# Optimization experiments

Measured on AMD Instinct MI355X. Metric: run time of the kernel, lower is better.

The kernel has to match this reference:

```python
import jax, jax.numpy as jnp
import numpy as np

D_MODEL = 1024
NUM_HEAD = 16
D_K = D_MODEL // NUM_HEAD
B, S = 2, 2048


def setup_inputs() -> dict:
    key = jax.random.key(0)
    ks = jax.random.split(key, 12)
    s = 1.0 / np.sqrt(D_MODEL)
    return {
        "x_q": jax.random.normal(ks[0], (B, S, D_MODEL), jnp.float32),
        "x_k": jax.random.normal(ks[1], (B, S, D_MODEL), jnp.float32),
        "x_v": jax.random.normal(ks[2], (B, S, D_MODEL), jnp.float32),
        "mask": jax.random.randint(ks[3], (B, S, S), 0, 2, jnp.int32),
        "Wq": jax.random.uniform(ks[4], (D_MODEL, D_MODEL), jnp.float32, -s, s),
        "bq": jax.random.uniform(ks[5], (D_MODEL,), jnp.float32, -s, s),
        "Wk": jax.random.uniform(ks[6], (D_MODEL, D_MODEL), jnp.float32, -s, s),
        "bk": jax.random.uniform(ks[7], (D_MODEL,), jnp.float32, -s, s),
        "Wv": jax.random.uniform(ks[8], (D_MODEL, D_MODEL), jnp.float32, -s, s),
        "bv": jax.random.uniform(ks[9], (D_MODEL,), jnp.float32, -s, s),
        "Wo": jax.random.uniform(ks[10], (D_MODEL, D_MODEL), jnp.float32, -s, s),
        "bo": jax.random.uniform(ks[11], (D_MODEL,), jnp.float32, -s, s),
    }


def reference(x_q, x_k, x_v, mask, Wq, bq, Wk, bk, Wv, bv, Wo, bo):
    # projections -> [B, H, S, d_k]
    def proj(x, W, b):
        y = x @ W.T + b
        return y.reshape(B, -1, NUM_HEAD, D_K).transpose(0, 2, 1, 3)

    q = proj(x_q, Wq, bq)
    k = proj(x_k, Wk, bk)
    v = proj(x_v, Wv, bv)
    scale = 1.0 / np.sqrt(D_K).astype(np.float32)
    scores = jnp.einsum("bhqd,bhkd->bhqk", q, k) * scale
    scores = jnp.where(mask[:, None, :, :] == 0, jnp.float32(-1e9), scores)
    p = jax.nn.softmax(scores, axis=-1)  # dropout is identity in eval mode
    attn = jnp.einsum("bhqk,bhkd->bhqd", p, v)
    concat = attn.transpose(0, 2, 1, 3).reshape(B, S, D_MODEL)
    return concat @ Wo.T + bo
```

## Files before the change

kernel.cpp:

```cpp
#include <hip/hip_runtime.h>
#include <cstdint>
#include <cstddef>

#define D_MODELX 1024
#define NUM_HEADX 16
#define D_KX 64
#define BBX 2
#define SSX 2048
#define M_TOK 4096
#define MBYTE (1u << 20)

typedef __attribute__((ext_vector_type(8))) short short8;
typedef __attribute__((ext_vector_type(4))) short short4v;
typedef __attribute__((ext_vector_type(4))) float float4v;
typedef __attribute__((ext_vector_type(2))) unsigned uint2v;
typedef __attribute__((ext_vector_type(4))) unsigned uint4v;

__device__ __forceinline__ short f2bf(float f) {
  unsigned u = __builtin_bit_cast(unsigned, f);
  u = u + 0x7FFFu + ((u >> 16) & 1u);
  return (short)(u >> 16);
}

__global__ void mask_bits_kernel(const int* __restrict__ mask, unsigned* __restrict__ mbits) {
  int i = blockIdx.x * blockDim.x + threadIdx.x;
  bool v = mask[i] != 0;
  unsigned long long bal = __ballot(v);
  int lane = threadIdx.x & 63;
  if (lane == 0)       mbits[i >> 5] = (unsigned)bal;
  else if (lane == 32) mbits[i >> 5] = (unsigned)(bal >> 32);
}

__global__ void cvt_w4_kernel(const float* __restrict__ w0, const float* __restrict__ w1,
                              const float* __restrict__ w2, const float* __restrict__ w3,
                              short* __restrict__ o0, short* __restrict__ o1,
                              short* __restrict__ o2, short* __restrict__ o3) {
  int z = blockIdx.y;
  const float* in = (z == 0) ? w0 : (z == 1) ? w1 : (z == 2) ? w2 : w3;
  short* out = (z == 0) ? o0 : (z == 1) ? o1 : (z == 2) ? o2 : o3;
  int i = blockIdx.x * blockDim.x + threadIdx.x;
  float4v v = ((const float4v*)in)[i];
  short4v s;
  s[0] = f2bf(v[0]); s[1] = f2bf(v[1]); s[2] = f2bf(v[2]); s[3] = f2bf(v[3]);
  ((short4v*)out)[i] = s;
}

__global__ void cvt_x3_kernel(const float* __restrict__ x0, const float* __restrict__ x1,
                              const float* __restrict__ x2,
                              short* __restrict__ o0, short* __restrict__ o1,
                              short* __restrict__ o2) {
  int z = blockIdx.y;
  const float* in = (z == 0) ? x0 : (z == 1) ? x1 : x2;
  short* out = (z == 0) ? o0 : (z == 1) ? o1 : o2;
  int i = blockIdx.x * blockDim.x + threadIdx.x;
  float4v v = ((const float4v*)in)[i];
  short4v s;
  s[0] = f2bf(v[0]); s[1] = f2bf(v[1]); s[2] = f2bf(v[2]); s[3] = f2bf(v[3]);
  ((short4v*)out)[i] = s;
}

#define GBK 64

__device__ __forceinline__ void gemm_body(const short* __restrict__ A,
                                          const short* __restrict__ Bw,
                                          const float* __restrict__ bias,
                                          float oscale, void* __restrict__ outp, int mode) {
  __shared__ short lds_a[128 * 64];
  __shared__ short lds_b[128 * 64];
  const int tid = threadIdx.x;
  const int lane = tid & 63;
  const int wid = tid >> 6;
  const int wm = wid >> 1, wn = wid & 1;
  const int bn = blockIdx.x, bm = blockIdx.y;
  const int l15 = lane & 15, lg = lane >> 4;

  const int s_row = tid >> 3;
  const int s_cB = ((tid & 7) << 4) ^ ((s_row & 7) << 4);
  const short* Abase = A + (size_t)(bm * 128) * 1024 + (s_cB >> 1);
  const short* Bbase = Bw + (size_t)(bn * 128) * 1024 + (s_cB >> 1);

  const int xmask = (l15 & 7) << 4;
  const int a_b0 = (wm * 64 + l15) * 128 + ((lg * 16) ^ xmask);
  const int a_b1 = (wm * 64 + l15) * 128 + ((64 + lg * 16) ^ xmask);
  const int b_b0 = (wn * 64 + l15) * 128 + ((lg * 16) ^ xmask);
  const int b_b1 = (wn * 64 + l15) * 128 + ((64 + lg * 16) ^ xmask);

  float4v acc[4][4];
#pragma unroll
  for (int m = 0; m < 4; ++m)
#pragma unroll
    for (int n = 0; n < 4; ++n) acc[m][n] = (float4v){0.f, 0.f, 0.f, 0.f};

  for (int kt = 0; kt < 1024; kt += GBK) {
#pragma unroll
    for (int it = 0; it < 4; ++it) {
      int row = it * 32 + s_row;
      __builtin_amdgcn_global_load_lds(
          (const uint32_t*)(Abase + (size_t)row * 1024 + kt),
          (uint32_t*)(lds_a + (it * 256 + wid * 64) * 8), 16, 0, 0);
      __builtin_amdgcn_global_load_lds(
          (const uint32_t*)(Bbase + (size_t)row * 1024 + kt),
          (uint32_t*)(lds_b + (it * 256 + wid * 64) * 8), 16, 0, 0);
    }
    __syncthreads();

    short8 af[4][2];
#pragma unroll
    for (int m = 0; m < 4; ++m) {
      af[m][0] = *(const short8*)((const char*)lds_a + a_b0 + m * 2048);
      af[m][1] = *(const short8*)((const char*)lds_a + a_b1 + m * 2048);
    }
#pragma unroll
    for (int n = 0; n < 4; ++n) {
      short8 b0 = *(const short8*)((const char*)lds_b + b_b0 + n * 2048);
      short8 b1 = *(const short8*)((const char*)lds_b + b_b1 + n * 2048);
#pragma unroll
      for (int m = 0; m < 4; ++m) {
        acc[m][n] = __builtin_amdgcn_mfma_f32_16x16x32_bf16(af[m][0], b0, acc[m][n], 0, 0, 0);
        acc[m][n] = __builtin_amdgcn_mfma_f32_16x16x32_bf16(af[m][1], b1, acc[m][n], 0, 0, 0);
      }
    }
    __syncthreads();
  }

#pragma unroll
  for (int n = 0; n < 4; ++n) {
    int col = bn * 128 + wn * 64 + n * 16 + l15;
    float bv = bias[col];
#pragma unroll
    for (int m = 0; m < 4; ++m) {
      if (mode == 2) {
        int base_row = bm * 128 + wm * 64 + m * 16 + lg * 4;
        int bidx = base_row >> 11, s = base_row & 2047;
        int h = col >> 6, d = col & 63;
        short4v sv;
#pragma unroll
        for (int r = 0; r < 4; ++r) sv[r] = f2bf(acc[m][n][r] + bv);
        *(short4v*)&((short*)outp)[(((size_t)(bidx * NUM_HEADX + h)) * D_KX + d) * SSX + s] = sv;
      } else {
#pragma unroll
        for (int r = 0; r < 4; ++r) {
          int row = bm * 128 + wm * 64 + m * 16 + lg * 4 + r;
          float val = (acc[m][n][r] + bv) * oscale;
          if (mode == 0) {
            int bidx = row >> 11, s = row & 2047;
            int h = col >> 6, d = col & 63;
            ((short*)outp)[(((size_t)(bidx * NUM_HEADX + h)) * SSX + s) * D_KX + d] = f2bf(val);
          } else {
            ((float*)outp)[(size_t)row * D_MODELX + col] = val;
          }
        }
      }
    }
  }
}

__global__ __launch_bounds__(256) void gemm_qkv_kernel(
    const short* __restrict__ xq, const short* __restrict__ xk, const short* __restrict__ xv,
    const short* __restrict__ wq, const short* __restrict__ wk, const short* __restrict__ wv,
    const float* __restrict__ bq, const float* __restrict__ bk, const float* __restrict__ bv,
    short* __restrict__ qo, short* __restrict__ ko, short* __restrict__ vo, float qs) {
  int z = blockIdx.z;
  const short* A = (z == 0) ? xq : (z == 1) ? xk : xv;
  const short* W = (z == 0) ? wq : (z == 1) ? wk : wv;
  const float* bi = (z == 0) ? bq : (z == 1) ? bk : bv;
  void* out = (z == 0) ? (void*)qo : (z == 1) ? (void*)ko : (void*)vo;
  float os = (z == 0) ? qs : 1.0f;
  int mode = (z == 2) ? 2 : 0;
  gemm_body(A, W, bi, os, out, mode);
}

__global__ __launch_bounds__(256) void gemm_one_kernel(const short* __restrict__ A,
                                                       const short* __restrict__ W,
                                                       const float* __restrict__ bias,
                                                       float os, void* __restrict__ out, int mode) {
  gemm_body(A, W, bias, os, out, mode);
}

__global__ __launch_bounds__(256, 3) void attn_kernel(const short* __restrict__ q_ws,
                                                      const short* __restrict__ k_ws,
                                                      const short* __restrict__ vT_ws,
                                                      const unsigned* __restrict__ mbits,
                                                      short* __restrict__ attn_ws,
                                                      short* __restrict__ opart,
                                                      float* __restrict__ lpart) {
  __shared__ short k_lds[2][4096];
  __shared__ short vT_lds[2][4096];
  __shared__ short p_lds[4][2048];

  const int tid = threadIdx.x;
  const int lane = tid & 63;
  const int w = tid >> 6;
  const int l15 = lane & 15, lg = lane >> 4;
  const int bid0 = blockIdx.x;
  const int bid = ((bid0 & 7) << 6) | (bid0 >> 3);
  const int qt = bid & 15;
  const int bh = bid >> 4;
  const int b = bh >> 4;
  const int h = bh & 15;
  const int z = blockIdx.z;
  const int nsplit = gridDim.z;
  const int nt = (SSX / 64) / nsplit;
  const int kb0 = z * nt * 64;

  const int qrow = qt * 128 + w * 32;

  const int xm15 = (l15 & 7) << 4;
  const int rd_c0 = l15 * 128 + ((lg * 16) ^ xm15);
  const int rd_c1 = l15 * 128 + ((64 + lg * 16) ^ xm15);
  char* kbase = (char*)k_lds;
  char* vbase = (char*)vT_lds;
  char* pwave = (char*)p_lds[w];
  const int s8 = ((l15 >> 2) & 3) << 3;
  const int pw_off = l15 * 32 + ((lg * 8) ^ s8);
  const int pr0 = (lg >> 1) * 512 + l15 * 32 + (((lg & 1) * 16) ^ s8);
  const int pr1 = pr0 ^ 8;

  const int srow = tid >> 2;
  const int scolS = (tid & 3) * 16;
  const int st0 = srow * 128 + ((scolS * 2) ^ ((srow & 7) << 4));
  const int st1 = srow * 128 + ((scolS * 2 + 16) ^ ((srow & 7) << 4));

  const short* kp = k_ws + (size_t)bh * SSX * D_KX + (size_t)srow * D_KX + scolS;
  const short* vp = vT_ws + (size_t)bh * D_KX * SSX + (size_t)srow * SSX + scolS;

  short8 qf[2][2];
#pragma unroll
  for (int qg = 0; qg < 2; ++qg)
#pragma unroll
    for (int c = 0; c < 2; ++c)
      qf[qg][c] = *(const short8*)(q_ws + ((size_t)bh * SSX + qrow + qg * 16 + l15) * D_KX + c * 32 + lg * 8);

  float4v acc[2][4];
#pragma unroll
  for (int qg = 0; qg < 2; ++qg)
#pragma unroll
    for (int db = 0; db < 4; ++db) acc[qg][db] = (float4v){0.f, 0.f, 0.f, 0.f};
  float l_part[2] = {0.f, 0.f};

  short8 kr0, kr1, vr0, vr1;
  auto loadt = [&](int kb) {
    const short* kq = kp + (size_t)kb * D_KX;
    kr0 = *(const short8*)kq;
    kr1 = *(const short8*)(kq + 8);
    const short* vq = vp + kb;
    vr0 = *(const short8*)vq;
    vr1 = *(const short8*)(vq + 8);
  };
  auto storet = [&](int BUF) {
    *(short8*)(kbase + BUF + st0) = kr0;
    *(short8*)(kbase + BUF + st1) = kr1;
    *(short8*)(vbase + BUF + st0) = vr0;
    *(short8*)(vbase + BUF + st1) = vr1;
  };

  const unsigned* mrow0 = mbits + ((size_t)b * SSX + qrow + l15) * (SSX / 32) + (kb0 >> 5);
  const unsigned* mrow1 = mbits + ((size_t)b * SSX + qrow + 16 + l15) * (SSX / 32) + (kb0 >> 5);
  unsigned long long mw0 = *(const unsigned long long*)mrow0, mwn0 = 0;
  unsigned long long mw1 = *(const unsigned long long*)mrow1, mwn1 = 0;

  loadt(kb0);
  storet(0);
  loadt(kb0 + 64);
  __syncthreads();

  auto step = [&](int t, int CURB, int NXTB) {
    float p[2][4][4];
#pragma unroll
    for (int kf = 0; kf < 4; ++kf) {
      short8 k0 = *(const short8*)(kbase + CURB + rd_c0 + kf * 2048);
      short8 k1 = *(const short8*)(kbase + CURB + rd_c1 + kf * 2048);
      float4v f0 = (float4v){0.f, 0.f, 0.f, 0.f};
      f0 = __builtin_amdgcn_mfma_f32_16x16x32_bf16(k0, qf[0][0], f0, 0, 0, 0);
      f0 = __builtin_amdgcn_mfma_f32_16x16x32_bf16(k1, qf[0][1], f0, 0, 0, 0);
      float4v f1 = (float4v){0.f, 0.f, 0.f, 0.f};
      f1 = __builtin_amdgcn_mfma_f32_16x16x32_bf16(k0, qf[1][0], f1, 0, 0, 0);
      f1 = __builtin_amdgcn_mfma_f32_16x16x32_bf16(k1, qf[1][1], f1, 0, 0, 0);
#pragma unroll
      for (int r = 0; r < 4; ++r) { p[0][kf][r] = f0[r]; p[1][kf][r] = f1[r]; }
    }

    if (t < nt - 1) storet(NXTB);
    if (t < nt - 2) loadt(kb0 + (t + 2) * 64);
    if (t < nt - 1) {
      mwn0 = *(const unsigned long long*)(mrow0 + 2 * (t + 1));
      mwn1 = *(const unsigned long long*)(mrow1 + 2 * (t + 1));
    }

#pragma unroll
    for (int qg = 0; qg < 2; ++qg) {
      unsigned long long sh = (qg == 0 ? mw0 : mw1) >> (lg * 4);
      unsigned mlo = (unsigned)sh, mhi = (unsigned)(sh >> 32);
      float tsum = 0.f;
#pragma unroll
      for (int kf = 0; kf < 4; ++kf) {
        float pv_[4];
#pragma unroll
        for (int r = 0; r < 4; ++r) {
          float pv = __builtin_amdgcn_exp2f(p[qg][kf][r]);
          unsigned bit = (kf < 2 ? mlo : mhi) & (1u << ((kf & 1) * 16 + r));
          pv_[r] = bit ? pv : 0.0f;
        }
        tsum += (pv_[0] + pv_[1]) + (pv_[2] + pv_[3]);
        unsigned u0, u1;
        asm("v_cvt_pk_bf16_f32 %0, %1, %2" : "=v"(u0) : "v"(pv_[0]), "v"(pv_[1]));
        asm("v_cvt_pk_bf16_f32 %0, %1, %2" : "=v"(u1) : "v"(pv_[2]), "v"(pv_[3]));
        *(uint2v*)(pwave + pw_off + qg * 2048 + kf * 512) = (uint2v){u0, u1};
      }
      l_part[qg] += tsum;
    }

    short8 pa[2][2];
#pragma unroll
    for (int qg = 0; qg < 2; ++qg)
#pragma unroll
      for (int c = 0; c < 2; ++c) {
        uint2v a0 = *(const uint2v*)(pwave + pr0 + qg * 2048 + c * 1024);
        uint2v a1 = *(const uint2v*)(pwave + pr1 + qg * 2048 + c * 1024);
        pa[qg][c] = __builtin_bit_cast(short8, (uint4v){a0[0], a0[1], a1[0], a1[1]});
      }

#pragma unroll
    for (int db = 0; db < 4; ++db) {
      short8 vb0 = *(const short8*)(vbase + CURB + rd_c0 + db * 2048);
      short8 vb1 = *(const short8*)(vbase + CURB + rd_c1 + db * 2048);
#pragma unroll
      for (int qg = 0; qg < 2; ++qg) {
        acc[qg][db] = __builtin_amdgcn_mfma_f32_16x16x32_bf16(vb0, pa[qg][0], acc[qg][db], 0, 0, 0);
        acc[qg][db] = __builtin_amdgcn_mfma_f32_16x16x32_bf16(vb1, pa[qg][1], acc[qg][db], 0, 0, 0);
      }
    }

    __syncthreads();
    mw0 = mwn0;
    mw1 = mwn1;
  };

  for (int t2 = 0; t2 < nt / 2; ++t2) {
    step(2 * t2, 0, 8192);
    step(2 * t2 + 1, 8192, 0);
  }

#pragma unroll
  for (int qg = 0; qg < 2; ++qg) {
    float lp = l_part[qg];
    lp += __shfl_xor(lp, 16);
    lp += __shfl_xor(lp, 32);
    const int q = qrow + qg * 16 + l15;
    if (nsplit == 1) {
      float inv = 1.0f / lp;
      size_t ttok = (size_t)b * SSX + q;
#pragma unroll
      for (int db = 0; db < 4; ++db) {
        short4v sv;
#pragma unroll
        for (int r = 0; r < 4; ++r) sv[r] = f2bf(acc[qg][db][r] * inv);
        *(short4v*)&attn_ws[ttok * D_MODELX + h * 64 + db * 16 + lg * 4] = sv;
      }
    } else {
      size_t rowp = ((size_t)z * 32 + bh) * SSX + q;
      if (lg == 0) lpart[rowp] = lp;
#pragma unroll
      for (int db = 0; db < 4; ++db) {
        short4v sv;
#pragma unroll
        for (int r = 0; r < 4; ++r) sv[r] = f2bf(acc[qg][db][r]);
        *(short4v*)&opart[rowp * D_KX + db * 16 + lg * 4] = sv;
      }
    }
  }
}

__global__ void combine_kernel(const short* __restrict__ opart, const float* __restrict__ lpart,
                               short* __restrict__ attn_ws) {
  int gtid = blockIdx.x * blockDim.x + threadIdx.x;
  int row = gtid >> 3;
  int dc = (gtid & 7) * 8;
  int bh = row >> 11, s = row & 2047;
  int b = bh >> 4, h = bh & 15;
  float inv = 1.0f / (lpart[row] + lpart[row + 32 * SSX]);
  short8 o0 = *(const short8*)&opart[(size_t)row * D_KX + dc];
  short8 o1 = *(const short8*)&opart[((size_t)row + 32 * SSX) * D_KX + dc];
  short8 sv;
#pragma unroll
  for (int j = 0; j < 8; ++j) {
    float f0 = __builtin_bit_cast(float, ((unsigned)(unsigned short)o0[j]) << 16);
    float f1 = __builtin_bit_cast(float, ((unsigned)(unsigned short)o1[j]) << 16);
    sv[j] = f2bf((f0 + f1) * inv);
  }
  *(short8*)&attn_ws[(((size_t)b * SSX + s) * D_MODELX) + h * 64 + dc] = sv;
}

extern "C" void kernel_launch(void* const* d_in, const int* in_sizes, int n_in,
                              void* d_out, int out_size, void* d_ws, size_t ws_size,
                              hipStream_t stream) {
  const float* x_q = (const float*)d_in[0];
  const float* x_k = (const float*)d_in[1];
  const float* x_v = (const float*)d_in[2];
  const int*   mask = (const int*)d_in[3];
  const float* Wq = (const float*)d_in[4];
  const float* bq = (const float*)d_in[5];
  const float* Wk = (const float*)d_in[6];
  const float* bk = (const float*)d_in[7];
  const float* Wv = (const float*)d_in[8];
  const float* bv = (const float*)d_in[9];
  const float* Wo = (const float*)d_in[10];
  const float* bo = (const float*)d_in[11];

  const float QSCALE = 0.125f * 1.44269504089f;

  char* ws = (char*)d_ws;
  short* q_ws  = (short*)(ws + 0 * MBYTE);
  short* k_ws  = (short*)(ws + 8 * MBYTE);
  short* vT_ws = (short*)(ws + 16 * MBYTE);

  dim3 ggrid(D_MODELX / 128, M_TOK / 128);

  if (ws_size >= (size_t)56 * MBYTE) {
    short* wq_bf = (short*)(ws + 24 * MBYTE);
    short* wk_bf = (short*)(ws + 26 * MBYTE);
    short* wv_bf = (short*)(ws + 28 * MBYTE);
    short* wo_bf = (short*)(ws + 30 * MBYTE);
    short* xq_bf = (short*)(ws + 32 * MBYTE);
    short* xk_bf = (short*)(ws + 40 * MBYTE);
    short* xv_bf = (short*)(ws + 48 * MBYTE);
    unsigned* mbits = (unsigned*)(ws + 24 * MBYTE);
    float* lpart    = (float*)(ws + 25 * MBYTE);
    short* attn_ws  = (short*)(ws + 32 * MBYTE);
    short* opart    = (short*)(ws + 40 * MBYTE);

    cvt_w4_kernel<<<dim3(1024, 4), 256, 0, stream>>>(Wq, Wk, Wv, Wo, wq_bf, wk_bf, wv_bf, wo_bf);
    cvt_x3_kernel<<<dim3(4096, 3), 256, 0, stream>>>(x_q, x_k, x_v, xq_bf, xk_bf, xv_bf);

    dim3 qkvgrid(D_MODELX / 128, M_TOK / 128, 3);
    gemm_qkv_kernel<<<qkvgrid, 256, 0, stream>>>(xq_bf, xk_bf, xv_bf, wq_bf, wk_bf, wv_bf,
                                                 bq, bk, bv, q_ws, k_ws, vT_ws, QSCALE);

    mask_bits_kernel<<<(BBX * SSX * SSX) / 256, 256, 0, stream>>>(mask, mbits);

    dim3 agrid(BBX * NUM_HEADX * (SSX / 128), 1, 2);
    attn_kernel<<<agrid, 256, 0, stream>>>(q_ws, k_ws, vT_ws, mbits, attn_ws, opart, lpart);
    combine_kernel<<<2048, 256, 0, stream>>>(opart, lpart, attn_ws);

    gemm_one_kernel<<<ggrid, 256, 0, stream>>>(attn_ws, wo_bf, bo, 1.0f, d_out, 1);
  } else {
    unsigned* mbits = (unsigned*)(ws + 24 * MBYTE);
    short* w_bf = (short*)(ws + 25 * MBYTE);
    short* x_bf = (short*)(ws + 27 * MBYTE);
    short* attn_ws = (short*)(ws + 27 * MBYTE);

    mask_bits_kernel<<<(BBX * SSX * SSX) / 256, 256, 0, stream>>>(mask, mbits);

    cvt_w4_kernel<<<dim3(1024, 1), 256, 0, stream>>>(Wq, Wq, Wq, Wq, w_bf, w_bf, w_bf, w_bf);
    cvt_x3_kernel<<<dim3(4096, 1), 256, 0, stream>>>(x_q, x_q, x_q, x_bf, x_bf, x_bf);
    gemm_one_kernel<<<ggrid, 256, 0, stream>>>(x_bf, w_bf, bq, QSCALE, q_ws, 0);

    cvt_w4_kernel<<<dim3(1024, 1), 256, 0, stream>>>(Wk, Wk, Wk, Wk, w_bf, w_bf, w_bf, w_bf);
    cvt_x3_kernel<<<dim3(4096, 1), 256, 0, stream>>>(x_k, x_k, x_k, x_bf, x_bf, x_bf);
    gemm_one_kernel<<<ggrid, 256, 0, stream>>>(x_bf, w_bf, bk, 1.0f, k_ws, 0);

    cvt_w4_kernel<<<dim3(1024, 1), 256, 0, stream>>>(Wv, Wv, Wv, Wv, w_bf, w_bf, w_bf, w_bf);
    cvt_x3_kernel<<<dim3(4096, 1), 256, 0, stream>>>(x_v, x_v, x_v, x_bf, x_bf, x_bf);
    gemm_one_kernel<<<ggrid, 256, 0, stream>>>(x_bf, w_bf, bv, 1.0f, vT_ws, 2);

    dim3 agrid(BBX * NUM_HEADX * (SSX / 128), 1, 1);
    attn_kernel<<<agrid, 256, 0, stream>>>(q_ws, k_ws, vT_ws, mbits, attn_ws, nullptr, nullptr);

    cvt_w4_kernel<<<dim3(1024, 1), 256, 0, stream>>>(Wo, Wo, Wo, Wo, w_bf, w_bf, w_bf, w_bf);
    gemm_one_kernel<<<ggrid, 256, 0, stream>>>(attn_ws, w_bf, bo, 1.0f, d_out, 1);
  }
}
```

Measured before the change: 165.1 us.

## Halve P scratch LDS, raise attention occupancy, add MFMA priority hints

The attention kernel now handles one 16-row query group at a time. P is written to LDS and its PV MFMAs run immediately, so the per-wave P buffer drops from 2048 to 1024 shorts. Less LDS per block, together with launch bounds raised from 3 to 4 blocks per CU, targets higher occupancy. s_setprio hints around the QK and PV MFMA sections try to interleave waves better. V fragments are loaded once for the first group and reused for the second, which may raise register pressure under the tighter occupancy limit and risks spills.

Measured after the change: 267.4 us. +62.0%, slower.

```diff
diff --git a/kernel.cpp b/kernel.cpp
--- a/kernel.cpp
+++ b/kernel.cpp
@@ -177,7 +177,7 @@
   gemm_body(A, W, bias, os, out, mode);
 }
 
-__global__ __launch_bounds__(256, 3) void attn_kernel(const short* __restrict__ q_ws,
+__global__ __launch_bounds__(256, 4) void attn_kernel(const short* __restrict__ q_ws,
                                                       const short* __restrict__ k_ws,
                                                       const short* __restrict__ vT_ws,
                                                       const unsigned* __restrict__ mbits,
@@ -186,7 +186,7 @@
                                                       float* __restrict__ lpart) {
   __shared__ short k_lds[2][4096];
   __shared__ short vT_lds[2][4096];
-  __shared__ short p_lds[4][2048];
+  __shared__ short p_lds[4][1024];
 
   const int tid = threadIdx.x;
   const int lane = tid & 63;
@@ -266,6 +266,7 @@
 
   auto step = [&](int t, int CURB, int NXTB) {
     float p[2][4][4];
+    __builtin_amdgcn_s_setprio(1);
 #pragma unroll
     for (int kf = 0; kf < 4; ++kf) {
       short8 k0 = *(const short8*)(kbase + CURB + rd_c0 + kf * 2048);
@@ -279,6 +280,7 @@
 #pragma unroll
       for (int r = 0; r < 4; ++r) { p[0][kf][r] = f0[r]; p[1][kf][r] = f1[r]; }
     }
+    __builtin_amdgcn_s_setprio(0);
 
     if (t < nt - 1) storet(NXTB);
     if (t < nt - 2) loadt(kb0 + (t + 2) * 64);
@@ -287,6 +289,7 @@
       mwn1 = *(const unsigned long long*)(mrow1 + 2 * (t + 1));
     }
 
+    short8 vb[4][2];
 #pragma unroll
     for (int qg = 0; qg < 2; ++qg) {
       unsigned long long sh = (qg == 0 ? mw0 : mw1) >> (lg * 4);
@@ -305,30 +308,31 @@
         unsigned u0, u1;
         asm("v_cvt_pk_bf16_f32 %0, %1, %2" : "=v"(u0) : "v"(pv_[0]), "v"(pv_[1]));
         asm("v_cvt_pk_bf16_f32 %0, %1, %2" : "=v"(u1) : "v"(pv_[2]), "v"(pv_[3]));
-        *(uint2v*)(pwave + pw_off + qg * 2048 + kf * 512) = (uint2v){u0, u1};
+        *(uint2v*)(pwave + pw_off + kf * 512) = (uint2v){u0, u1};
       }
       l_part[qg] += tsum;
-    }
-
-    short8 pa[2][2];
-#pragma unroll
-    for (int qg = 0; qg < 2; ++qg)
-#pragma unroll
-      for (int c = 0; c < 2; ++c) {
-        uint2v a0 = *(const uint2v*)(pwave + pr0 + qg * 2048 + c * 1024);
-        uint2v a1 = *(const uint2v*)(pwave + pr1 + qg * 2048 + c * 1024);
-        pa[qg][c] = __builtin_bit_cast(short8, (uint4v){a0[0], a0[1], a1[0], a1[1]});
-      }
-
-#pragma unroll
-    for (int db = 0; db < 4; ++db) {
-      short8 vb0 = *(const short8*)(vbase + CURB + rd_c0 + db * 2048);
-      short8 vb1 = *(const short8*)(vbase + CURB + rd_c1 + db * 2048);
-#pragma unroll
-      for (int qg = 0; qg < 2; ++qg) {
-        acc[qg][db] = __builtin_amdgcn_mfma_f32_16x16x32_bf16(vb0, pa[qg][0], acc[qg][db], 0, 0, 0);
-        acc[qg][db] = __builtin_amdgcn_mfma_f32_16x16x32_bf16(vb1, pa[qg][1], acc[qg][db], 0, 0, 0);
-      }
+
+      short8 pa0, pa1;
+      {
+        uint2v a0 = *(const uint2v*)(pwave + pr0);
+        uint2v a1 = *(const uint2v*)(pwave + pr1);
+        pa0 = __builtin_bit_cast(short8, (uint4v){a0[0], a0[1], a1[0], a1[1]});
+        uint2v b0 = *(const uint2v*)(pwave + pr0 + 1024);
+        uint2v b1 = *(const uint2v*)(pwave + pr1 + 1024);
+        pa1 = __builtin_bit_cast(short8, (uint4v){b0[0], b0[1], b1[0], b1[1]});
+      }
+
+      __builtin_amdgcn_s_setprio(1);
+#pragma unroll
+      for (int db = 0; db < 4; ++db) {
+        if (qg == 0) {
+          vb[db][0] = *(const short8*)(vbase + CURB + rd_c0 + db * 2048);
+          vb[db][1] = *(const short8*)(vbase + CURB + rd_c1 + db * 2048);
+        }
+        acc[qg][db] = __builtin_amdgcn_mfma_f32_16x16x32_bf16(vb[db][0], pa0, acc[qg][db], 0, 0, 0);
+        acc[qg][db] = __builtin_amdgcn_mfma_f32_16x16x32_bf16(vb[db][1], pa1, acc[qg][db], 0, 0, 0);
+      }
+      __builtin_amdgcn_s_setprio(0);
     }
 
     __syncthreads();
```
